# Kernel tuning notes

Measured on AMD Instinct MI355X. Metric: run time of the kernel, lower is better.

The kernel has to match this reference:

```python
import math
import jax, jax.numpy as jnp
import numpy as np

SDE_THRESHOLD = 10.0
ANGLE_THRESHOLD_DEG = 30.0


def setup_inputs() -> dict:
    key = jax.random.key(0)
    k1, k2 = jax.random.split(key)
    B, H, N = 8, 16, 1024
    y_pred = jax.random.normal(k1, (B, H, 4), dtype=jnp.float32)
    sample_points = jax.random.normal(k2, (B, N, 3), dtype=jnp.float32)
    return {"y_pred": y_pred, "sample_points": sample_points}


def reference(y_pred, sample_points):
    # y_pred: [B,H,4] = (nx,ny,nz,d) per plane head; sample_points: [B,N,3]
    B, H, _ = y_pred.shape
    n = y_pred[..., :3]
    n = n / jnp.linalg.norm(n, axis=-1, keepdims=True)  # normalize normals
    d = y_pred[..., 3]

    # transform_representation_cm: represent plane by (normal, point) where
    # point = projection of the point-cloud centroid onto the plane n.x + d = 0
    cm = sample_points.mean(axis=1)  # [B,3]
    point = cm[:, None, :] - (jnp.einsum('bhd,bd->bh', n, cm) + d)[..., None] * n  # [B,H,3]

    # chamfer_adapter: reflect points across each plane, bidirectional chamfer (squared dists)
    proj = jnp.einsum('bnd,bhd->bhn', sample_points, n) + d[:, :, None]  # [B,H,N]
    refl = sample_points[:, None, :, :] - 2.0 * proj[..., None] * n[:, :, None, :]  # [B,H,N,3]
    rr = jnp.sum(refl * refl, axis=-1)                  # [B,H,N]
    ss = jnp.sum(sample_points * sample_points, axis=-1)  # [B,N]
    cross = jnp.einsum('bhid,bjd->bhij', refl, sample_points)  # [B,H,N,N]
    d2 = rr[..., None] + ss[:, None, None, :] - 2.0 * cross
    sde = jnp.min(d2, axis=-1).mean(axis=-1) + jnp.min(d2, axis=-2).mean(axis=-1)  # [B,H]

    # minmax_normalization -> confidence = 1 - (sde - min) / |max - min| per batch row
    mn = sde.min(axis=1, keepdims=True)
    mx = sde.max(axis=1, keepdims=True)
    conf = 1.0 - (sde - mn) / jnp.abs(mx - mn)

    # pairwise angle-based duplicate suppression (vectorized NMS)
    cos = jnp.clip(jnp.einsum('bhd,bgd->bhg', n, n), -1.0, 1.0)
    ang = jnp.arccos(cos) * (180.0 / math.pi)
    close = (ang < ANGLE_THRESHOLD_DEG) | (180.0 - ang < ANGLE_THRESHOLD_DEG)
    close = close & ~jnp.eye(H, dtype=bool)
    valid = sde <= SDE_THRESHOLD  # filter x.sde <= sde_threshold
    # plane i is popped iff exists valid j (close) with sde_i >= sde_j (equal sde pops both)
    sup = valid & jnp.any(close & valid[:, None, :] & (sde[:, :, None] >= sde[:, None, :]), axis=-1)
    keep = valid & ~sup

    # to_tensor(): [normal(3), point(3), confidence, sde]; sort kept by confidence desc,
    # zero-pad suppressed/filtered slots (fixed shape [B,H,8] instead of ragged pad_sequence)
    planes = jnp.concatenate([n, point, conf[..., None], sde[..., None]], axis=-1)  # [B,H,8]
    sort_key = jnp.where(keep, conf, -jnp.inf)
    order = jnp.argsort(-sort_key, axis=1)
    planes_s = jnp.take_along_axis(planes, order[..., None], axis=1)
    keep_s = jnp.take_along_axis(keep, order, axis=1)
    return jnp.where(keep_s[..., None], planes_s, 0.0)
```

## Files before the change

### kernel.cpp

```cpp
#include <hip/hip_runtime.h>
#include <math.h>

#define BB 8
#define HH 16
#define NN 1024
#define TB 256


__global__ __launch_bounds__(TB) void chamfer_kernel(
    const float* __restrict__ y_pred,
    const float* __restrict__ sp,
    float* __restrict__ ws)
{
    __shared__ __align__(16) float4 pts[NN];
    __shared__ float wsum[4];

    const int blk = blockIdx.x;
    const int bh  = blk >> 2;
    const int q   = blk & 3;
    const int b   = bh >> 4;
    const int tid = threadIdx.x;

    float pnx = y_pred[bh * 4 + 0];
    float pny = y_pred[bh * 4 + 1];
    float pnz = y_pred[bh * 4 + 2];
    float pd  = y_pred[bh * 4 + 3];
    float inv = 1.0f / sqrtf(pnx * pnx + pny * pny + pnz * pnz);
    pnx *= inv; pny *= inv; pnz *= inv;

    const float* spb = sp + (size_t)b * NN * 3;

    for (int k = tid; k < NN; k += TB) {
        float x = spb[k * 3 + 0], y = spb[k * 3 + 1], z = spb[k * 3 + 2];
        pts[k] = make_float4(x, y, z, x * x + y * y + z * z);
    }

    float mx, my, mz, osq;
    {
        int i = q * TB + tid;
        float x = spb[i * 3 + 0], y = spb[i * 3 + 1], z = spb[i * 3 + 2];
        float proj = x * pnx + y * pny + z * pnz + pd;
        x -= 2.0f * proj * pnx;
        y -= 2.0f * proj * pny;
        z -= 2.0f * proj * pnz;
        osq = x * x + y * y + z * z;
        mx = -2.0f * x; my = -2.0f * y; mz = -2.0f * z;
    }
    __syncthreads();

    float m0 = 3.4e38f, m1 = 3.4e38f;

#define DIST(qq) fmaf(mx, qq.x, fmaf(my, qq.y, fmaf(mz, qq.z, qq.w)))
    for (int j = 0; j < NN; j += 8) {
        float4 q0 = pts[j + 0];
        float4 q1 = pts[j + 1];
        float4 q2 = pts[j + 2];
        float4 q3 = pts[j + 3];
        float4 q4 = pts[j + 4];
        float4 q5 = pts[j + 5];
        float4 q6 = pts[j + 6];
        float4 q7 = pts[j + 7];
        float d0 = DIST(q0), d1 = DIST(q1), d2 = DIST(q2), d3 = DIST(q3);
        float d4 = DIST(q4), d5 = DIST(q5), d6 = DIST(q6), d7 = DIST(q7);
        m0 = fminf(fminf(m0, d0), d1);
        m1 = fminf(fminf(m1, d2), d3);
        m0 = fminf(fminf(m0, d4), d5);
        m1 = fminf(fminf(m1, d6), d7);
    }
#undef DIST

    float dmin = osq + fminf(m0, m1);

    float s = dmin;
    for (int off = 32; off; off >>= 1) s += __shfl_down(s, off, 64);
    if ((tid & 63) == 0) wsum[tid >> 6] = s;
    __syncthreads();
    if (tid == 0)
        ws[bh * 4 + q] = (wsum[0] + wsum[1]) + (wsum[2] + wsum[3]);
}

__global__ __launch_bounds__(TB) void finalize_kernel(
    const float* __restrict__ ws,
    const float* __restrict__ y_pred,
    const float* __restrict__ sp,
    float* __restrict__ out)
{
    const int b   = blockIdx.x;
    const int tid = threadIdx.x;

    __shared__ float sde_s[HH], nx_s[HH], ny_s[HH], nz_s[HH], d_s[HH], conf_s[HH];
    __shared__ float cmacc[3];
    __shared__ int keep_s[HH];

    if (tid < 3) cmacc[tid] = 0.0f;
    __syncthreads();

    const float* spb = sp + (size_t)b * NN * 3;
    float sx = 0.0f, sy = 0.0f, sz = 0.0f;
    for (int p = tid; p < NN; p += TB) {
        sx += spb[p * 3 + 0];
        sy += spb[p * 3 + 1];
        sz += spb[p * 3 + 2];
    }
    for (int off = 32; off; off >>= 1) {
        sx += __shfl_down(sx, off, 64);
        sy += __shfl_down(sy, off, 64);
        sz += __shfl_down(sz, off, 64);
    }
    if ((tid & 63) == 0) {
        atomicAdd(&cmacc[0], sx);
        atomicAdd(&cmacc[1], sy);
        atomicAdd(&cmacc[2], sz);
    }
    __syncthreads();

    const float cmx = cmacc[0] / NN, cmy = cmacc[1] / NN, cmz = cmacc[2] / NN;

    if (tid < HH) {
        int h = tid;
        float nx = y_pred[(b * HH + h) * 4 + 0];
        float ny = y_pred[(b * HH + h) * 4 + 1];
        float nz = y_pred[(b * HH + h) * 4 + 2];
        float d  = y_pred[(b * HH + h) * 4 + 3];
        float inv = 1.0f / sqrtf(nx * nx + ny * ny + nz * nz);
        nx *= inv; ny *= inv; nz *= inv;
        nx_s[h] = nx; ny_s[h] = ny; nz_s[h] = nz; d_s[h] = d;
        const float* w = ws + (size_t)(b * HH + h) * 4;
        sde_s[h] = ((w[0] + w[1]) + (w[2] + w[3])) * (2.0f / NN);
    }
    __syncthreads();

    if (tid < HH) {
        int h = tid;
        float mn = sde_s[0], mx = sde_s[0];
        for (int g = 1; g < HH; ++g) {
            mn = fminf(mn, sde_s[g]);
            mx = fmaxf(mx, sde_s[g]);
        }
        float sde  = sde_s[h];
        float conf = 1.0f - (sde - mn) / fabsf(mx - mn);
        conf_s[h]  = conf;
        bool valid = (sde <= 10.0f);
        bool sup   = false;
        if (valid) {
            for (int g = 0; g < HH; ++g) {
                if (g == h) continue;
                float c = nx_s[h] * nx_s[g] + ny_s[h] * ny_s[g] + nz_s[h] * nz_s[g];
                c = fminf(1.0f, fmaxf(-1.0f, c));
                float ang = acosf(c) * 57.29577951308232f;
                bool close = (ang < 30.0f) || (180.0f - ang < 30.0f);
                if (close && (sde_s[g] <= 10.0f) && (sde >= sde_s[g])) sup = true;
            }
        }
        keep_s[h] = (valid && !sup) ? 1 : 0;
    }
    __syncthreads();

    if (tid < HH) {
        int h = tid;
        float keyh = keep_s[h] ? conf_s[h] : -INFINITY;
        int pos = 0;
        for (int g = 0; g < HH; ++g) {
            float keyg = keep_s[g] ? conf_s[g] : -INFINITY;
            if (keyg > keyh || (keyg == keyh && g < h)) ++pos;
        }
        float nx = nx_s[h], ny = ny_s[h], nz = nz_s[h];
        float t  = nx * cmx + ny * cmy + nz * cmz + d_s[h];
        float px = cmx - t * nx, py = cmy - t * ny, pz = cmz - t * nz;

        float* o = out + (size_t)(b * HH + pos) * 8;
        if (keep_s[h]) {
            o[0] = nx; o[1] = ny; o[2] = nz;
            o[3] = px; o[4] = py; o[5] = pz;
            o[6] = conf_s[h];
            o[7] = sde_s[h];
        } else {
            for (int c = 0; c < 8; ++c) o[c] = 0.0f;
        }
    }
}

extern "C" void kernel_launch(void* const* d_in, const int* in_sizes, int n_in,
                              void* d_out, int out_size, void* d_ws, size_t ws_size,
                              hipStream_t stream) {
    const float* y_pred = (const float*)d_in[0];
    const float* sp     = (const float*)d_in[1];
    float* out          = (float*)d_out;
    float* ws           = (float*)d_ws;

    chamfer_kernel<<<dim3(BB * HH * 4), dim3(TB), 0, stream>>>(y_pred, sp, ws);
    finalize_kernel<<<dim3(BB), dim3(TB), 0, stream>>>(ws, y_pred, sp, out);
}
```

Measured before the change: 78.54 us.

## Prepack points in global memory and stream them via scalar loads

Adds a pack kernel that writes (x,y,z,|p|^2) float4s to workspace once per batch. The chamfer kernel drops its per-block LDS staging and barrier and instead reads the packed points through inline-asm s_load_dwordx16 scalar loads, which are wave-uniform and broadcast to all lanes. This removes redundant repacking and LDS traffic per block. In exchange it adds a kernel launch and waits on lgkmcnt(0) every iteration, which serializes the scalar memory latency with no prefetch.

```diff
diff --git a/kernel.cpp b/kernel.cpp
--- a/kernel.cpp
+++ b/kernel.cpp
@@ -5,14 +5,25 @@
 #define HH 16
 #define NN 1024
 #define TB 256
-
+#define PACKF (BB * NN * 4)
+
+typedef float f32x16 __attribute__((ext_vector_type(16)));
+
+
+__global__ __launch_bounds__(TB) void pack_kernel(
+    const float* __restrict__ sp,
+    float* __restrict__ ws)
+{
+    int idx = blockIdx.x * TB + threadIdx.x;
+    float x = sp[idx * 3 + 0], y = sp[idx * 3 + 1], z = sp[idx * 3 + 2];
+    ((float4*)ws)[idx] = make_float4(x, y, z, x * x + y * y + z * z);
+}
 
 __global__ __launch_bounds__(TB) void chamfer_kernel(
     const float* __restrict__ y_pred,
     const float* __restrict__ sp,
     float* __restrict__ ws)
 {
-    __shared__ __align__(16) float4 pts[NN];
     __shared__ float wsum[4];
 
     const int blk = blockIdx.x;
@@ -28,12 +39,7 @@
     float inv = 1.0f / sqrtf(pnx * pnx + pny * pny + pnz * pnz);
     pnx *= inv; pny *= inv; pnz *= inv;
 
-    const float* spb = sp + (size_t)b * NN * 3;
-
-    for (int k = tid; k < NN; k += TB) {
-        float x = spb[k * 3 + 0], y = spb[k * 3 + 1], z = spb[k * 3 + 2];
-        pts[k] = make_float4(x, y, z, x * x + y * y + z * z);
-    }
+    const float* __restrict__ spb = sp + (size_t)b * NN * 3;
 
     float mx, my, mz, osq;
     {
@@ -46,22 +52,28 @@
         osq = x * x + y * y + z * z;
         mx = -2.0f * x; my = -2.0f * y; mz = -2.0f * z;
     }
-    __syncthreads();
 
     float m0 = 3.4e38f, m1 = 3.4e38f;
 
-#define DIST(qq) fmaf(mx, qq.x, fmaf(my, qq.y, fmaf(mz, qq.z, qq.w)))
-    for (int j = 0; j < NN; j += 8) {
-        float4 q0 = pts[j + 0];
-        float4 q1 = pts[j + 1];
-        float4 q2 = pts[j + 2];
-        float4 q3 = pts[j + 3];
-        float4 q4 = pts[j + 4];
-        float4 q5 = pts[j + 5];
-        float4 q6 = pts[j + 6];
-        float4 q7 = pts[j + 7];
-        float d0 = DIST(q0), d1 = DIST(q1), d2 = DIST(q2), d3 = DIST(q3);
-        float d4 = DIST(q4), d5 = DIST(q5), d6 = DIST(q6), d7 = DIST(q7);
+    const float* p = ws + (size_t)b * NN * 4;
+
+#define DIST(X, Y, Z, W) fmaf(mx, X, fmaf(my, Y, fmaf(mz, Z, W)))
+    for (int j = 0; j < NN; j += 8, p += 32) {
+        f32x16 A, B;
+        asm volatile(
+            "s_load_dwordx16 %0, %2, 0\n\t"
+            "s_load_dwordx16 %1, %2, 64\n\t"
+            "s_waitcnt lgkmcnt(0)"
+            : "=&s"(A), "=&s"(B)
+            : "s"(p));
+        float d0 = DIST(A[0],  A[1],  A[2],  A[3]);
+        float d1 = DIST(A[4],  A[5],  A[6],  A[7]);
+        float d2 = DIST(A[8],  A[9],  A[10], A[11]);
+        float d3 = DIST(A[12], A[13], A[14], A[15]);
+        float d4 = DIST(B[0],  B[1],  B[2],  B[3]);
+        float d5 = DIST(B[4],  B[5],  B[6],  B[7]);
+        float d6 = DIST(B[8],  B[9],  B[10], B[11]);
+        float d7 = DIST(B[12], B[13], B[14], B[15]);
         m0 = fminf(fminf(m0, d0), d1);
         m1 = fminf(fminf(m1, d2), d3);
         m0 = fminf(fminf(m0, d4), d5);
@@ -76,7 +88,7 @@
     if ((tid & 63) == 0) wsum[tid >> 6] = s;
     __syncthreads();
     if (tid == 0)
-        ws[bh * 4 + q] = (wsum[0] + wsum[1]) + (wsum[2] + wsum[3]);
+        ws[PACKF + bh * 4 + q] = (wsum[0] + wsum[1]) + (wsum[2] + wsum[3]);
 }
 
 __global__ __launch_bounds__(TB) void finalize_kernel(
@@ -125,7 +137,7 @@
         float inv = 1.0f / sqrtf(nx * nx + ny * ny + nz * nz);
         nx *= inv; ny *= inv; nz *= inv;
         nx_s[h] = nx; ny_s[h] = ny; nz_s[h] = nz; d_s[h] = d;
-        const float* w = ws + (size_t)(b * HH + h) * 4;
+        const float* w = ws + PACKF + (size_t)(b * HH + h) * 4;
         sde_s[h] = ((w[0] + w[1]) + (w[2] + w[3])) * (2.0f / NN);
     }
     __syncthreads();
@@ -188,6 +200,7 @@
     float* out          = (float*)d_out;
     float* ws           = (float*)d_ws;
 
+    pack_kernel<<<dim3(BB * NN / TB), dim3(TB), 0, stream>>>(sp, ws);
     chamfer_kernel<<<dim3(BB * HH * 4), dim3(TB), 0, stream>>>(y_pred, sp, ws);
     finalize_kernel<<<dim3(BB), dim3(TB), 0, stream>>>(ws, y_pred, sp, out);
 }
```

Measured after the change: 102.0 us. +29.8%, slower.

## Register-block four queries per thread and split candidate scan across waves

Applied to the files above, without the earlier changes.

Each thread now holds four reflected query points in registers, and each wavefront scans only a 256-point chunk of the shared candidate set instead of all 1024. The per-wave partial minima are combined through a shared-memory array before the sum reduction. This lets every shared-memory float4 load feed four distance computations instead of one, cutting LDS traffic per FMA. In exchange it uses more registers and an extra shared buffer plus a barrier to merge the partial minima.

```diff
diff --git a/kernel.cpp b/kernel.cpp
--- a/kernel.cpp
+++ b/kernel.cpp
@@ -5,6 +5,7 @@
 #define HH 16
 #define NN 1024
 #define TB 256
+#define SCH 256
 
 
 __global__ __launch_bounds__(TB) void chamfer_kernel(
@@ -13,6 +14,7 @@
     float* __restrict__ ws)
 {
     __shared__ __align__(16) float4 pts[NN];
+    __shared__ float part[4][SCH];
     __shared__ float wsum[4];
 
     const int blk = blockIdx.x;
@@ -20,6 +22,8 @@
     const int q   = blk & 3;
     const int b   = bh >> 4;
     const int tid = threadIdx.x;
+    const int w   = tid >> 6;
+    const int l   = tid & 63;
 
     float pnx = y_pred[bh * 4 + 0];
     float pny = y_pred[bh * 4 + 1];
@@ -28,52 +32,66 @@
     float inv = 1.0f / sqrtf(pnx * pnx + pny * pny + pnz * pnz);
     pnx *= inv; pny *= inv; pnz *= inv;
 
-    const float* spb = sp + (size_t)b * NN * 3;
+    const float* __restrict__ spb = sp + (size_t)b * NN * 3;
 
     for (int k = tid; k < NN; k += TB) {
         float x = spb[k * 3 + 0], y = spb[k * 3 + 1], z = spb[k * 3 + 2];
         pts[k] = make_float4(x, y, z, x * x + y * y + z * z);
     }
-
-    float mx, my, mz, osq;
-    {
-        int i = q * TB + tid;
-        float x = spb[i * 3 + 0], y = spb[i * 3 + 1], z = spb[i * 3 + 2];
+    __syncthreads();
+
+    float mx[4], my[4], mz[4], osq[4];
+#pragma unroll
+    for (int u = 0; u < 4; ++u) {
+        float4 P = pts[q * SCH + l + 64 * u];
+        float x = P.x, y = P.y, z = P.z;
         float proj = x * pnx + y * pny + z * pnz + pd;
         x -= 2.0f * proj * pnx;
         y -= 2.0f * proj * pny;
         z -= 2.0f * proj * pnz;
-        osq = x * x + y * y + z * z;
-        mx = -2.0f * x; my = -2.0f * y; mz = -2.0f * z;
-    }
-    __syncthreads();
-
-    float m0 = 3.4e38f, m1 = 3.4e38f;
-
-#define DIST(qq) fmaf(mx, qq.x, fmaf(my, qq.y, fmaf(mz, qq.z, qq.w)))
-    for (int j = 0; j < NN; j += 8) {
-        float4 q0 = pts[j + 0];
-        float4 q1 = pts[j + 1];
-        float4 q2 = pts[j + 2];
-        float4 q3 = pts[j + 3];
-        float4 q4 = pts[j + 4];
-        float4 q5 = pts[j + 5];
-        float4 q6 = pts[j + 6];
-        float4 q7 = pts[j + 7];
-        float d0 = DIST(q0), d1 = DIST(q1), d2 = DIST(q2), d3 = DIST(q3);
-        float d4 = DIST(q4), d5 = DIST(q5), d6 = DIST(q6), d7 = DIST(q7);
-        m0 = fminf(fminf(m0, d0), d1);
-        m1 = fminf(fminf(m1, d2), d3);
-        m0 = fminf(fminf(m0, d4), d5);
-        m1 = fminf(fminf(m1, d6), d7);
+        osq[u] = x * x + y * y + z * z;
+        mx[u] = -2.0f * x; my[u] = -2.0f * y; mz[u] = -2.0f * z;
+    }
+
+    float m0[4], m1[4];
+#pragma unroll
+    for (int u = 0; u < 4; ++u) { m0[u] = 3.4e38f; m1[u] = 3.4e38f; }
+
+    const float4* __restrict__ chunk = pts + w * SCH;
+
+#define DIST(qq, u) fmaf(mx[u], qq.x, fmaf(my[u], qq.y, fmaf(mz[u], qq.z, qq.w)))
+    for (int j = 0; j < SCH; j += 4) {
+        float4 q0 = chunk[j + 0];
+        float4 q1 = chunk[j + 1];
+        float4 q2 = chunk[j + 2];
+        float4 q3 = chunk[j + 3];
+#pragma unroll
+        for (int u = 0; u < 4; ++u) {
+            float d0 = DIST(q0, u);
+            float d1 = DIST(q1, u);
+            float d2 = DIST(q2, u);
+            float d3 = DIST(q3, u);
+            m0[u] = fminf(fminf(m0[u], d0), d1);
+            m1[u] = fminf(fminf(m1[u], d2), d3);
+        }
     }
 #undef DIST
 
-    float dmin = osq + fminf(m0, m1);
+#pragma unroll
+    for (int u = 0; u < 4; ++u)
+        part[w][l + 64 * u] = fminf(m0[u], m1[u]);
+    __syncthreads();
+
+    float p0 = part[0][tid], p1 = part[1][tid];
+    float p2 = part[2][tid], p3 = part[3][tid];
+    float cmin = fminf(fminf(p0, p1), fminf(p2, p3));
+    float osq_own = (w == 0) ? osq[0] : (w == 1) ? osq[1]
+                  : (w == 2) ? osq[2] : osq[3];
+    float dmin = osq_own + cmin;
 
     float s = dmin;
     for (int off = 32; off; off >>= 1) s += __shfl_down(s, off, 64);
-    if ((tid & 63) == 0) wsum[tid >> 6] = s;
+    if (l == 0) wsum[w] = s;
     __syncthreads();
     if (tid == 0)
         ws[bh * 4 + q] = (wsum[0] + wsum[1]) + (wsum[2] + wsum[3]);
```

Result: faster. 73.52 us (-6.4%).
